# Performance work log

Measured on AMD Instinct MI355X. Metric: run time of the kernel, lower is better.

The kernel has to match this reference:

```python
import jax, jax.numpy as jnp
import numpy as np

B, S, D_MODEL, NHEAD = 2, 2048, 2048, 16
HEAD_DIM = D_MODEL // NHEAD
FREQ = 10000.0


def rope(x, freq):
    # x: [B, S, D] -- rotary applied over the FULL projection dim (pre head-split),
    # interleaved pairs (even, odd), theta_i = freq^(-2i/D)
    S_, D = x.shape[-2], x.shape[-1]
    half = D // 2
    inv_freq = freq ** (-(jnp.arange(half, dtype=jnp.float32) * 2.0) / D)  # [D/2]
    ang = jnp.arange(S_, dtype=jnp.float32)[:, None] * inv_freq[None, :]   # [S, D/2]
    cos, sin = jnp.cos(ang), jnp.sin(ang)
    x1, x2 = x[..., 0::2], x[..., 1::2]
    r1 = x1 * cos - x2 * sin
    r2 = x1 * sin + x2 * cos
    return jnp.stack([r1, r2], axis=-1).reshape(x.shape)


def split_heads(x, h):
    b, s, d = x.shape
    return x.reshape(b, s, h, d // h).transpose(0, 2, 1, 3)  # [B,H,S,Dh]


def setup_inputs() -> dict:
    key = jax.random.key(0)
    ks = jax.random.split(key, 9)
    sc = 1.0 / np.sqrt(D_MODEL)
    inp = {
        "queries": jax.random.normal(ks[0], (B, S, D_MODEL), dtype=jnp.float32),
        "key_attention_mask": jnp.ones((B, S), dtype=bool),
        "wq": jax.random.normal(ks[1], (D_MODEL, D_MODEL), dtype=jnp.float32) * sc,
        "bq": jnp.zeros((D_MODEL,), dtype=jnp.float32),
        "wk": jax.random.normal(ks[2], (D_MODEL, D_MODEL), dtype=jnp.float32) * sc,
        "bk": jnp.zeros((D_MODEL,), dtype=jnp.float32),
        "wv": jax.random.normal(ks[3], (D_MODEL, D_MODEL), dtype=jnp.float32) * sc,
        "bv": jnp.zeros((D_MODEL,), dtype=jnp.float32),
        "wo": jax.random.normal(ks[4], (D_MODEL, D_MODEL), dtype=jnp.float32) * sc,
        "bo": jnp.zeros((D_MODEL,), dtype=jnp.float32),
    }
    return inp


def reference(queries, key_attention_mask, wq, bq, wk, bk, wv, bv, wo, bo):
    # self-attention: values = keys = queries
    q_proj = queries @ wq.T + bq
    k_proj = queries @ wk.T + bk
    v_proj = queries @ wv.T + bv

    Q = split_heads(rope(q_proj, FREQ), NHEAD)   # [B,H,S,Dh]
    K = split_heads(rope(k_proj, FREQ), NHEAD)
    V = split_heads(v_proj, NHEAD)

    scale = 1.0 / np.sqrt(HEAD_DIM)
    scores = jnp.einsum("bhqd,bhkd->bhqk", Q, K) * scale  # [B,H,S,S]
    mask = key_attention_mask[:, None, None, :]            # [B,1,1,S] True = attend
    scores = jnp.where(mask, scores, jnp.float32(-1e30))
    attn = jax.nn.softmax(scores, axis=-1)
    heads = jnp.einsum("bhqk,bhkd->bhqd", attn, V)         # [B,H,S,Dh]

    out = heads.transpose(0, 2, 1, 3).reshape(B, S, D_MODEL)
    return out @ wo.T + bo
```

## Files before the change

### kernel.cpp

```cpp
#include <hip/hip_runtime.h>
#include <hip/hip_fp16.h>

typedef _Float16 f16;
typedef _Float16 f16x8 __attribute__((ext_vector_type(8)));
typedef _Float16 f16x4 __attribute__((ext_vector_type(4)));
typedef float    f32x4 __attribute__((ext_vector_type(4)));

__device__ __forceinline__ void gload16(const void* g, void* l) {
  __builtin_amdgcn_global_load_lds(
      (__attribute__((address_space(1))) void*)(g),
      (__attribute__((address_space(3))) void*)(l), 16, 0, 0);
}

__device__ __forceinline__ void rope_sincos(float ang, float* sn, float* cs) {
  float rev = ang * 0.15915494309189535f;
  rev = rev - floorf(rev);
  const float a = rev * 6.283185307179586f;
  *sn = __sinf(a);
  *cs = __cosf(a);
}

struct Cvt6 {
  const float* src[6];
  f16* dst[6];
};
__global__ __launch_bounds__(256) void cvt6(Cvt6 a) {
  const int seg = blockIdx.y;
  const size_t i = (size_t)blockIdx.x * 256 + threadIdx.x;
  float4 v = ((const float4*)a.src[seg])[i];
  f16x4 o;
  o[0] = (f16)v.x; o[1] = (f16)v.y; o[2] = (f16)v.z; o[3] = (f16)v.w;
  ((f16x4*)a.dst[seg])[i] = o;
}

template <int BN, bool SPLIT3, bool OUT_F16>
__global__ __launch_bounds__(256) void gemm_bt(
    const f16* __restrict__ A, const f16* __restrict__ Bw,
    const float* __restrict__ b0, const float* __restrict__ b1, const float* __restrict__ b2,
    void* __restrict__ o0, void* __restrict__ o1, void* __restrict__ o2,
    int M, int Ntot, int K) {
  constexpr int NT = BN / 32;
  __shared__ f16 As[128 * 32];
  __shared__ f16 Bs[BN * 32];
  const int tid = threadIdx.x;
  const int wave = tid >> 6, lane = tid & 63;
  const int lane15 = lane & 15, quad = lane >> 4;
  const int wm = wave >> 1, wn = wave & 1;
  const int m0 = blockIdx.x * 128, n0 = blockIdx.y * BN;
  const int srow = tid >> 2;
  const int skc = ((tid & 3) ^ ((srow >> 1) & 3)) * 8;
  const f16* ga = A + (size_t)(m0 + srow) * K + skc;
  const f16* gb = Bw + (size_t)(n0 + srow) * K + skc;
  f16* lA = As + wave * 512;
  f16* lB = Bs + wave * 512;
  const int fsw = (lane15 >> 1) & 3;

  f32x4 acc[4][NT] = {};
  for (int k0 = 0; k0 < K; k0 += 32) {
    gload16(ga + k0, lA);
    gload16(ga + (size_t)64 * K + k0, lA + 2048);
#pragma unroll
    for (int p = 0; p < BN / 64; p++)
      gload16(gb + (size_t)(p * 64) * K + k0, lB + p * 2048);
    __syncthreads();
    f16x8 af[4], bf[NT];
#pragma unroll
    for (int mt = 0; mt < 4; mt++)
      af[mt] = *(const f16x8*)(As + (wm * 64 + mt * 16 + lane15) * 32 + ((quad ^ fsw) * 8));
#pragma unroll
    for (int nt = 0; nt < NT; nt++)
      bf[nt] = *(const f16x8*)(Bs + (wn * (BN / 2) + nt * 16 + lane15) * 32 + ((quad ^ fsw) * 8));
#pragma unroll
    for (int mt = 0; mt < 4; mt++)
#pragma unroll
      for (int nt = 0; nt < NT; nt++)
        acc[mt][nt] = __builtin_amdgcn_mfma_f32_16x16x32_f16(af[mt], bf[nt], acc[mt][nt], 0, 0, 0);
    __syncthreads();
  }
#pragma unroll
  for (int nt = 0; nt < NT; nt++) {
    const int col = n0 + wn * (BN / 2) + nt * 16 + lane15;
    if (SPLIT3) {
      const int which = col >> 11;
      const int ocol = col & 2047;
      if (which == 2) {
        const float bias = b2[ocol];
#pragma unroll
        for (int mt = 0; mt < 4; mt++) {
          const int row = m0 + wm * 64 + mt * 16 + quad * 4;
          const int bb = row >> 11, s = row & 2047;
          f16x4 pk;
#pragma unroll
          for (int r = 0; r < 4; r++) pk[r] = (f16)(acc[mt][nt][r] + bias);
          *(f16x4*)((f16*)o2 + (((size_t)bb * 2048 + ocol) * 2048 + s)) = pk;
        }
      } else {
        const float bias = (which == 0) ? b0[ocol] : b1[ocol];
        f16* op = (f16*)((which == 0) ? o0 : o1);
        const float inv = expf((float)(ocol >> 1) * (-9.210340371976184f / 1024.f));
        const float sgn = (ocol & 1) ? 1.f : -1.f;
#pragma unroll
        for (int mt = 0; mt < 4; mt++) {
          const int row = m0 + wm * 64 + mt * 16 + quad * 4;
#pragma unroll
          for (int r = 0; r < 4; r++) {
            const float x = acc[mt][nt][r] + bias;
            const float xp = __shfl_xor(x, 1, 64);
            const int s = (row + r) & 2047;
            float sn, cs;
            rope_sincos((float)s * inv, &sn, &cs);
            op[(size_t)(row + r) * 2048 + ocol] = (f16)(x * cs + sgn * (xp * sn));
          }
        }
      }
    } else {
      const float bias = b0[col];
#pragma unroll
      for (int mt = 0; mt < 4; mt++) {
        const int row = m0 + wm * 64 + mt * 16 + quad * 4;
#pragma unroll
        for (int r = 0; r < 4; r++) {
          const float v = acc[mt][nt][r] + bias;
          if (OUT_F16)
            ((f16*)o0)[(size_t)(row + r) * Ntot + col] = (f16)v;
          else
            ((float*)o0)[(size_t)(row + r) * Ntot + col] = v;
        }
      }
    }
  }
}

__global__ __launch_bounds__(256) void flash_attn(
    const f16* __restrict__ Q, const f16* __restrict__ Kg,
    const f16* __restrict__ Vt, f16* __restrict__ Hout) {
  constexpr int S = 2048, DM = 2048, HD = 128, KT = 64, NTI = S / KT;
  __shared__ f16 Ks[2][KT * HD];
  __shared__ f16 Vs[2][HD * KT];
  const int tid = threadIdx.x;
  const int wave = tid >> 6, lane = tid & 63;
  const int lane15 = lane & 15, quad = lane >> 4;
  const int qt = blockIdx.x, bh = blockIdx.y;
  const int b = bh >> 4, h = bh & 15;
  const float cexp = 0.12751744f;

  const size_t qkbase = (size_t)b * S * DM + (size_t)h * HD;
  const size_t vbase = ((size_t)b * DM + (size_t)h * HD) * S;

  f16x8 qf[2][4];
#pragma unroll
  for (int mt = 0; mt < 2; mt++) {
    const int qrow = qt * 128 + wave * 32 + mt * 16 + lane15;
#pragma unroll
    for (int kt = 0; kt < 4; kt++)
      qf[mt][kt] = *(const f16x8*)(Q + qkbase + (size_t)qrow * DM + kt * 32 + quad * 8);
  }

  f32x4 o[2][8] = {};
  float lp[2] = {};

  const int krow = tid >> 4;
  const int kkc = ((tid & 15) ^ krow) * 8;
  const int vrow = tid >> 3;
  const int vkc = ((tid & 7) ^ (vrow & 7)) * 8;
  const f16* gK = Kg + qkbase;
  const f16* gV = Vt + vbase;

  auto issue_loads = [&](int s0, int nb) {
#pragma unroll
    for (int p = 0; p < 4; p++)
      gload16(gK + (size_t)(s0 + p * 16 + krow) * DM + kkc, &Ks[nb][wave * 512] + p * 2048);
#pragma unroll
    for (int p = 0; p < 4; p++)
      gload16(gV + (size_t)(p * 32 + vrow) * S + s0 + vkc, &Vs[nb][wave * 512] + p * 2048);
  };

  issue_loads(0, 0);

  for (int it = 0; it < NTI; it++) {
    const int buf = it & 1;
    __syncthreads();
    if (it + 1 < NTI) issue_loads((it + 1) * KT, buf ^ 1);

    f32x4 sf[4][2] = {};
#pragma unroll
    for (int ktd = 0; ktd < 4; ktd++) {
      f16x8 af[4];
#pragma unroll
      for (int kt = 0; kt < 4; kt++)
        af[kt] = *(const f16x8*)(&Ks[buf][(kt * 16 + lane15) * HD + (((ktd * 4 + quad) ^ lane15) * 8)]);
#pragma unroll
      for (int kt = 0; kt < 4; kt++)
#pragma unroll
        for (int mt = 0; mt < 2; mt++)
          sf[kt][mt] = __builtin_amdgcn_mfma_f32_16x16x32_f16(af[kt], qf[mt][ktd], sf[kt][mt], 0, 0, 0);
    }

    f16x4 pf[4][2];
#pragma unroll
    for (int kt = 0; kt < 4; kt++)
#pragma unroll
      for (int mt = 0; mt < 2; mt++)
#pragma unroll
        for (int r = 0; r < 4; r++) {
          const float p = __builtin_amdgcn_exp2f(sf[kt][mt][r] * cexp);
          lp[mt] += p;
          pf[kt][mt][r] = (f16)p;
        }

#pragma unroll
    for (int dt = 0; dt < 8; dt++) {
#pragma unroll
      for (int kt = 0; kt < 4; kt++) {
        const int chunk = kt * 2 + (quad >> 1);
        const f16x4 vf = *(const f16x4*)(
            &Vs[buf][(dt * 16 + lane15) * KT + (((chunk ^ (lane15 & 7)) << 3) | ((quad & 1) * 4))]);
#pragma unroll
        for (int mt = 0; mt < 2; mt++)
          o[mt][dt] = __builtin_amdgcn_mfma_f32_16x16x16f16(pf[kt][mt], vf, o[mt][dt], 0, 0, 0);
      }
    }
  }

#pragma unroll
  for (int mt = 0; mt < 2; mt++) {
    lp[mt] += __shfl_xor(lp[mt], 16, 64);
    lp[mt] += __shfl_xor(lp[mt], 32, 64);
  }
#pragma unroll
  for (int mt = 0; mt < 2; mt++)
#pragma unroll
    for (int r = 0; r < 4; r++) {
      const float inv = 1.f / __shfl(lp[mt], quad * 4 + r, 64);
      const int qrow = qt * 128 + wave * 32 + mt * 16 + quad * 4 + r;
#pragma unroll
      for (int dt = 0; dt < 8; dt++)
        Hout[qkbase + (size_t)qrow * DM + dt * 16 + lane15] = (f16)(o[mt][dt][r] * inv);
    }
}

extern "C" void kernel_launch(void* const* d_in, const int* in_sizes, int n_in,
                              void* d_out, int out_size, void* d_ws, size_t ws_size,
                              hipStream_t stream) {
  const float* qx = (const float*)d_in[0];
  const float* wq = (const float*)d_in[2];
  const float* bq = (const float*)d_in[3];
  const float* wk = (const float*)d_in[4];
  const float* bk = (const float*)d_in[5];
  const float* wv = (const float*)d_in[6];
  const float* bv = (const float*)d_in[7];
  const float* wo = (const float*)d_in[8];
  const float* bo = (const float*)d_in[9];
  float* out = (float*)d_out;

  constexpr int B = 2, S = 2048, DM = 2048;
  constexpr size_t XEL = (size_t)B * S * DM;
  constexpr size_t WEL = (size_t)DM * DM;

  f16* Xh  = (f16*)d_ws;
  f16* Wqh = Xh + XEL;
  f16* Wkh = Wqh + WEL;
  f16* Wvh = Wkh + WEL;
  f16* Woh = Wvh + WEL;
  f16* Qp  = Woh + WEL;
  f16* Kp  = Qp + XEL;
  f16* Vt  = Kp + XEL;
  f16* Hd  = Xh;

  Cvt6 c;
  c.src[0] = qx; c.src[1] = qx + XEL / 2;
  c.src[2] = wq; c.src[3] = wk; c.src[4] = wv; c.src[5] = wo;
  c.dst[0] = Xh; c.dst[1] = Xh + XEL / 2;
  c.dst[2] = Wqh; c.dst[3] = Wkh; c.dst[4] = Wvh; c.dst[5] = Woh;
  dim3 gcvt((unsigned)(WEL / 4 / 256), 6);
  cvt6<<<gcvt, 256, 0, stream>>>(c);

  dim3 gqkv(4096 / 128, 6144 / 128);
  gemm_bt<128, true, true><<<gqkv, 256, 0, stream>>>(Xh, Wqh, bq, bk, bv, Qp, Kp, Vt,
                                                     4096, 6144, 2048);

  dim3 gfa(16, 32);
  flash_attn<<<gfa, 256, 0, stream>>>(Qp, Kp, Vt, Hd);

  dim3 gout(4096 / 128, 2048 / 128);
  gemm_bt<128, false, false><<<gout, 256, 0, stream>>>(Hd, Woh, bo, nullptr, nullptr,
                                                       out, nullptr, nullptr,
                                                       4096, 2048, 2048);
}
```

Baseline: 432.3 us.

## Split attention over two key halves with combine kernel; smaller output GEMM tile

The flash attention grid gains a z-dimension that splits the key sequence into two halves. Each half writes an unnormalized partial output and its row sums, and a new combine kernel adds the two partials and normalizes them. This doubles the attention block count from 512 to 1024 so the GPU's compute units are better filled. The V buffer goes from double- to single-buffered, with extra barriers per tile. The output projection now uses 64-row M tiles for more blocks, at the cost of an extra kernel launch and extra partial-output memory traffic.

Measured after the change: 443.2 us. 1.03x slower.

```diff
diff --git a/kernel.cpp b/kernel.cpp
--- a/kernel.cpp
+++ b/kernel.cpp
@@ -33,20 +33,20 @@
   ((f16x4*)a.dst[seg])[i] = o;
 }
 
-template <int BN, bool SPLIT3, bool OUT_F16>
+template <int BM, int BN, bool SPLIT3, bool OUT_F16>
 __global__ __launch_bounds__(256) void gemm_bt(
     const f16* __restrict__ A, const f16* __restrict__ Bw,
     const float* __restrict__ b0, const float* __restrict__ b1, const float* __restrict__ b2,
     void* __restrict__ o0, void* __restrict__ o1, void* __restrict__ o2,
     int M, int Ntot, int K) {
-  constexpr int NT = BN / 32;
-  __shared__ f16 As[128 * 32];
+  constexpr int NT = BN / 32, MT = BM / 32;
+  __shared__ f16 As[BM * 32];
   __shared__ f16 Bs[BN * 32];
   const int tid = threadIdx.x;
   const int wave = tid >> 6, lane = tid & 63;
   const int lane15 = lane & 15, quad = lane >> 4;
   const int wm = wave >> 1, wn = wave & 1;
-  const int m0 = blockIdx.x * 128, n0 = blockIdx.y * BN;
+  const int m0 = blockIdx.x * BM, n0 = blockIdx.y * BN;
   const int srow = tid >> 2;
   const int skc = ((tid & 3) ^ ((srow >> 1) & 3)) * 8;
   const f16* ga = A + (size_t)(m0 + srow) * K + skc;
@@ -55,23 +55,24 @@
   f16* lB = Bs + wave * 512;
   const int fsw = (lane15 >> 1) & 3;
 
-  f32x4 acc[4][NT] = {};
+  f32x4 acc[MT][NT] = {};
   for (int k0 = 0; k0 < K; k0 += 32) {
-    gload16(ga + k0, lA);
-    gload16(ga + (size_t)64 * K + k0, lA + 2048);
+#pragma unroll
+    for (int p = 0; p < BM / 64; p++)
+      gload16(ga + (size_t)(p * 64) * K + k0, lA + p * 2048);
 #pragma unroll
     for (int p = 0; p < BN / 64; p++)
       gload16(gb + (size_t)(p * 64) * K + k0, lB + p * 2048);
     __syncthreads();
-    f16x8 af[4], bf[NT];
-#pragma unroll
-    for (int mt = 0; mt < 4; mt++)
-      af[mt] = *(const f16x8*)(As + (wm * 64 + mt * 16 + lane15) * 32 + ((quad ^ fsw) * 8));
+    f16x8 af[MT], bf[NT];
+#pragma unroll
+    for (int mt = 0; mt < MT; mt++)
+      af[mt] = *(const f16x8*)(As + (wm * (BM / 2) + mt * 16 + lane15) * 32 + ((quad ^ fsw) * 8));
 #pragma unroll
     for (int nt = 0; nt < NT; nt++)
       bf[nt] = *(const f16x8*)(Bs + (wn * (BN / 2) + nt * 16 + lane15) * 32 + ((quad ^ fsw) * 8));
 #pragma unroll
-    for (int mt = 0; mt < 4; mt++)
+    for (int mt = 0; mt < MT; mt++)
 #pragma unroll
       for (int nt = 0; nt < NT; nt++)
         acc[mt][nt] = __builtin_amdgcn_mfma_f32_16x16x32_f16(af[mt], bf[nt], acc[mt][nt], 0, 0, 0);
@@ -86,8 +87,8 @@
       if (which == 2) {
         const float bias = b2[ocol];
 #pragma unroll
-        for (int mt = 0; mt < 4; mt++) {
-          const int row = m0 + wm * 64 + mt * 16 + quad * 4;
+        for (int mt = 0; mt < MT; mt++) {
+          const int row = m0 + wm * (BM / 2) + mt * 16 + quad * 4;
           const int bb = row >> 11, s = row & 2047;
           f16x4 pk;
 #pragma unroll
@@ -100,8 +101,8 @@
         const float inv = expf((float)(ocol >> 1) * (-9.210340371976184f / 1024.f));
         const float sgn = (ocol & 1) ? 1.f : -1.f;
 #pragma unroll
-        for (int mt = 0; mt < 4; mt++) {
-          const int row = m0 + wm * 64 + mt * 16 + quad * 4;
+        for (int mt = 0; mt < MT; mt++) {
+          const int row = m0 + wm * (BM / 2) + mt * 16 + quad * 4;
 #pragma unroll
           for (int r = 0; r < 4; r++) {
             const float x = acc[mt][nt][r] + bias;
@@ -116,8 +117,8 @@
     } else {
       const float bias = b0[col];
 #pragma unroll
-      for (int mt = 0; mt < 4; mt++) {
-        const int row = m0 + wm * 64 + mt * 16 + quad * 4;
+      for (int mt = 0; mt < MT; mt++) {
+        const int row = m0 + wm * (BM / 2) + mt * 16 + quad * 4;
 #pragma unroll
         for (int r = 0; r < 4; r++) {
           const float v = acc[mt][nt][r] + bias;
@@ -133,15 +134,17 @@
 
 __global__ __launch_bounds__(256) void flash_attn(
     const f16* __restrict__ Q, const f16* __restrict__ Kg,
-    const f16* __restrict__ Vt, f16* __restrict__ Hout) {
-  constexpr int S = 2048, DM = 2048, HD = 128, KT = 64, NTI = S / KT;
+    const f16* __restrict__ Vt, f16* __restrict__ O0, f16* __restrict__ O1,
+    float* __restrict__ L) {
+  constexpr int S = 2048, DM = 2048, HD = 128, KT = 64, NTI = 1024 / KT;
   __shared__ f16 Ks[2][KT * HD];
-  __shared__ f16 Vs[2][HD * KT];
+  __shared__ f16 Vs[HD * KT];
   const int tid = threadIdx.x;
   const int wave = tid >> 6, lane = tid & 63;
   const int lane15 = lane & 15, quad = lane >> 4;
-  const int qt = blockIdx.x, bh = blockIdx.y;
+  const int qt = blockIdx.x, bh = blockIdx.y, kh = blockIdx.z;
   const int b = bh >> 4, h = bh & 15;
+  const int sbase = kh * 1024;
   const float cexp = 0.12751744f;
 
   const size_t qkbase = (size_t)b * S * DM + (size_t)h * HD;
@@ -166,21 +169,24 @@
   const f16* gK = Kg + qkbase;
   const f16* gV = Vt + vbase;
 
-  auto issue_loads = [&](int s0, int nb) {
+  auto issueK = [&](int s0, int nb) {
 #pragma unroll
     for (int p = 0; p < 4; p++)
-      gload16(gK + (size_t)(s0 + p * 16 + krow) * DM + kkc, &Ks[nb][wave * 512] + p * 2048);
+      gload16(gK + (size_t)(sbase + s0 + p * 16 + krow) * DM + kkc, &Ks[nb][wave * 512] + p * 2048);
+  };
+  auto issueV = [&](int s0) {
 #pragma unroll
     for (int p = 0; p < 4; p++)
-      gload16(gV + (size_t)(p * 32 + vrow) * S + s0 + vkc, &Vs[nb][wave * 512] + p * 2048);
+      gload16(gV + (size_t)(p * 32 + vrow) * S + sbase + s0 + vkc, Vs + wave * 512 + p * 2048);
   };
 
-  issue_loads(0, 0);
+  issueK(0, 0);
+  __syncthreads();
 
   for (int it = 0; it < NTI; it++) {
     const int buf = it & 1;
-    __syncthreads();
-    if (it + 1 < NTI) issue_loads((it + 1) * KT, buf ^ 1);
+    issueV(it * KT);
+    if (it + 1 < NTI) issueK((it + 1) * KT, buf ^ 1);
 
     f32x4 sf[4][2] = {};
 #pragma unroll
@@ -208,18 +214,21 @@
           pf[kt][mt][r] = (f16)p;
         }
 
+    __syncthreads();
+
 #pragma unroll
     for (int dt = 0; dt < 8; dt++) {
 #pragma unroll
       for (int kt = 0; kt < 4; kt++) {
         const int chunk = kt * 2 + (quad >> 1);
         const f16x4 vf = *(const f16x4*)(
-            &Vs[buf][(dt * 16 + lane15) * KT + (((chunk ^ (lane15 & 7)) << 3) | ((quad & 1) * 4))]);
+            &Vs[(dt * 16 + lane15) * KT + (((chunk ^ (lane15 & 7)) << 3) | ((quad & 1) * 4))]);
 #pragma unroll
         for (int mt = 0; mt < 2; mt++)
           o[mt][dt] = __builtin_amdgcn_mfma_f32_16x16x16f16(pf[kt][mt], vf, o[mt][dt], 0, 0, 0);
       }
     }
+    __syncthreads();
   }
 
 #pragma unroll
@@ -227,16 +236,37 @@
     lp[mt] += __shfl_xor(lp[mt], 16, 64);
     lp[mt] += __shfl_xor(lp[mt], 32, 64);
   }
-#pragma unroll
-  for (int mt = 0; mt < 2; mt++)
+  f16* Op = kh ? O1 : O0;
+#pragma unroll
+  for (int mt = 0; mt < 2; mt++) {
+    if (quad == 0)
+      L[(((size_t)kh * 32 + bh) << 11) + qt * 128 + wave * 32 + mt * 16 + lane15] = lp[mt];
 #pragma unroll
     for (int r = 0; r < 4; r++) {
-      const float inv = 1.f / __shfl(lp[mt], quad * 4 + r, 64);
       const int qrow = qt * 128 + wave * 32 + mt * 16 + quad * 4 + r;
 #pragma unroll
       for (int dt = 0; dt < 8; dt++)
-        Hout[qkbase + (size_t)qrow * DM + dt * 16 + lane15] = (f16)(o[mt][dt][r] * inv);
+        Op[qkbase + (size_t)qrow * DM + dt * 16 + lane15] = (f16)o[mt][dt][r];
     }
+  }
+}
+
+__global__ __launch_bounds__(256) void combine2(
+    const f16* __restrict__ O0, const f16* __restrict__ O1,
+    const float* __restrict__ L, f16* __restrict__ Hd) {
+  const size_t i = (size_t)blockIdx.x * 256 + threadIdx.x;
+  const size_t x8 = i * 8;
+  const int b = (int)(x8 >> 22);
+  const int s = (int)(x8 >> 11) & 2047;
+  const int h = (int)(x8 >> 7) & 15;
+  const int lidx = ((b * 16 + h) << 11) + s;
+  const float inv = 1.f / (L[lidx] + L[65536 + lidx]);
+  const f16x8 a = *(const f16x8*)(O0 + x8);
+  const f16x8 c = *(const f16x8*)(O1 + x8);
+  f16x8 o;
+#pragma unroll
+  for (int j = 0; j < 8; j++) o[j] = (f16)(((float)a[j] + (float)c[j]) * inv);
+  *(f16x8*)(Hd + x8) = o;
 }
 
 extern "C" void kernel_launch(void* const* d_in, const int* in_sizes, int n_in,
@@ -265,7 +295,10 @@
   f16* Qp  = Woh + WEL;
   f16* Kp  = Qp + XEL;
   f16* Vt  = Kp + XEL;
-  f16* Hd  = Xh;
+  f16* O0 = Xh;
+  f16* O1 = Wqh;
+  float* Lbuf = (float*)Wvh;
+  f16* Hd = Xh;
 
   Cvt6 c;
   c.src[0] = qx; c.src[1] = qx + XEL / 2;
@@ -276,14 +309,16 @@
   cvt6<<<gcvt, 256, 0, stream>>>(c);
 
   dim3 gqkv(4096 / 128, 6144 / 128);
-  gemm_bt<128, true, true><<<gqkv, 256, 0, stream>>>(Xh, Wqh, bq, bk, bv, Qp, Kp, Vt,
-                                                     4096, 6144, 2048);
-
-  dim3 gfa(16, 32);
-  flash_attn<<<gfa, 256, 0, stream>>>(Qp, Kp, Vt, Hd);
-
-  dim3 gout(4096 / 128, 2048 / 128);
-  gemm_bt<128, false, false><<<gout, 256, 0, stream>>>(Hd, Woh, bo, nullptr, nullptr,
-                                                       out, nullptr, nullptr,
-                                                       4096, 2048, 2048);
-}
+  gemm_bt<128, 128, true, true><<<gqkv, 256, 0, stream>>>(Xh, Wqh, bq, bk, bv, Qp, Kp, Vt,
+                                                          4096, 6144, 2048);
+
+  dim3 gfa(16, 32, 2);
+  flash_attn<<<gfa, 256, 0, stream>>>(Qp, Kp, Vt, O0, O1, Lbuf);
+
+  combine2<<<(unsigned)(XEL / 8 / 256), 256, 0, stream>>>(O0, O1, Lbuf, Hd);
+
+  dim3 gout(4096 / 64, 2048 / 128);
+  gemm_bt<64, 128, false, false><<<gout, 256, 0, stream>>>(Hd, Woh, bo, nullptr, nullptr,
+                                                           out, nullptr, nullptr,
+                                                           4096, 2048, 2048);
+}
```
